# Performance work log

Measured on AMD Instinct MI355X. Metric: run time of the kernel, lower is better.

Reference implementation:

```python
import jax, jax.numpy as jnp
import numpy as np

C = 256
CQK = C // 8  # 32

def setup_inputs() -> dict:
    key = jax.random.key(0)
    ks = jax.random.split(key, 8)
    B, H, W = 8, 64, 64
    x = jax.random.normal(ks[0], (B, C, H, W), dtype=jnp.float32)
    y = jax.random.normal(ks[1], (B, C, H, W), dtype=jnp.float32)
    s = 1.0 / np.sqrt(C)
    Wq = jax.random.normal(ks[2], (CQK, C), dtype=jnp.float32) * s
    bq = jnp.zeros((CQK,), dtype=jnp.float32)
    Wk = jax.random.normal(ks[3], (CQK, C), dtype=jnp.float32) * s
    bk = jnp.zeros((CQK,), dtype=jnp.float32)
    Wv = jax.random.normal(ks[4], (C, C), dtype=jnp.float32) * s
    bv = jnp.zeros((C,), dtype=jnp.float32)
    return {"x": x, "y": y, "Wq": Wq, "bq": bq, "Wk": Wk, "bk": bk, "Wv": Wv, "bv": bv}

def reference(x, y, Wq, bq, Wk, bk, Wv, bv):
    B, Cc, H, W = x.shape
    HW = H * W
    xf = x.reshape(B, Cc, HW)  # [B,C,HW]
    yf = y.reshape(B, Cc, HW)
    # 1x1 convs == per-pixel linear projections
    Q = jnp.einsum('oc,bcn->bno', Wq, xf) + bq          # [B,HW,CQK]
    K = jnp.einsum('oc,bcn->bon', Wk, yf) + bk[:, None]  # [B,CQK,HW]
    V = jnp.einsum('oc,bcn->bon', Wv, yf) + bv[:, None]  # [B,C,HW]
    attn = jax.nn.softmax(jnp.einsum('bnd,bdm->bnm', Q, K), axis=-1)  # [B,HW,HW]
    out = jnp.einsum('bcm,bnm->bcn', V, attn)  # V @ attn^T -> [B,C,HW]
    return out.reshape(B, Cc, H, W)
```

## Files before the change

kernel.cpp:

```cpp
#include <hip/hip_runtime.h>

typedef unsigned short u16;
typedef _Float16 f16;
typedef __attribute__((ext_vector_type(8))) short v8s;
typedef __attribute__((ext_vector_type(4))) short v4s;
typedef __attribute__((ext_vector_type(8))) f16   v8h;
typedef __attribute__((ext_vector_type(4))) float v4f;
typedef __attribute__((ext_vector_type(16))) float v16f;
typedef __attribute__((ext_vector_type(4))) unsigned v4u;

#define NB   8
#define NC   256
#define DQK  32
#define NPIX 4096

__device__ __forceinline__ u16 f2bf(float f) {
  unsigned u = __builtin_bit_cast(unsigned, f);
  u += 0x7FFFu + ((u >> 16) & 1u);
  return (u16)(u >> 16);
}
__device__ __forceinline__ u16 f2h(float f) {
  return __builtin_bit_cast(u16, (f16)f);
}
__device__ __forceinline__ unsigned cvt_pk_bf16(float lo, float hi) {
  unsigned r;
  asm("v_cvt_pk_bf16_f32 %0, %1, %2" : "=v"(r) : "v"(lo), "v"(hi));
  return r;
}
__device__ __forceinline__ float fast_exp2(float x) {
  float r;
  asm("v_exp_f32 %0, %1" : "=v"(r) : "v"(x));
  return r;
}

__global__ __launch_bounds__(256)
void convert_w(const float* __restrict__ Wq, const float* __restrict__ Wk,
               const float* __restrict__ Wv,
               u16* __restrict__ Whq, u16* __restrict__ Whk, u16* __restrict__ Whv) {
  int i = blockIdx.x * 256 + threadIdx.x;
  if (i < 8192)       Whq[i]         = f2h(Wq[i]);
  else if (i < 16384) Whk[i - 8192]  = f2h(Wk[i - 8192]);
  else                Whv[i - 16384] = f2h(Wv[i - 16384]);
}

__global__ __launch_bounds__(256, 2)
void proj_direct(const float* __restrict__ x, const float* __restrict__ y,
                 const u16* __restrict__ Whq, const float* __restrict__ bq,
                 const u16* __restrict__ Whk, const float* __restrict__ bk,
                 const u16* __restrict__ Whv, const float* __restrict__ bv,
                 u16* __restrict__ Qb, u16* __restrict__ Kb, u16* __restrict__ Vt) {
  const int tid = threadIdx.x, w = tid >> 6, lane = tid & 63;
  const int lr = lane & 15, quad = lane >> 4;
  const int b = blockIdx.x & 7;
  const int n0 = (blockIdx.x >> 3) * 64;
  const int n = n0 + w * 16 + lr;
  const size_t bn = ((size_t)b << 12) + n;

  const float* __restrict__ xp = x + ((size_t)b << 20) + n;
  const float* __restrict__ yp = y + ((size_t)b << 20) + n;

  v4f aq[2], ak[2], av[16];
#pragma unroll
  for (int ot = 0; ot < 2; ++ot) { aq[ot] = (v4f){0.f,0.f,0.f,0.f}; ak[ot] = (v4f){0.f,0.f,0.f,0.f}; }
#pragma unroll
  for (int vt = 0; vt < 16; ++vt) av[vt] = (v4f){0.f,0.f,0.f,0.f};

#pragma unroll
  for (int cs = 0; cs < 4; ++cs) {
    v8h xb0, xb1, yb0, yb1;
#pragma unroll
    for (int j = 0; j < 8; ++j) {
      const size_t c0 = (size_t)(cs * 64 + quad * 8 + j) * NPIX;
      const size_t c1 = (size_t)(cs * 64 + 32 + quad * 8 + j) * NPIX;
      xb0[j] = (f16)xp[c0];
      xb1[j] = (f16)xp[c1];
      yb0[j] = (f16)yp[c0];
      yb1[j] = (f16)yp[c1];
    }

#pragma unroll
    for (int ot = 0; ot < 2; ++ot) {
      const u16* wqp = Whq + (ot * 16 + lr) * 256 + cs * 64 + quad * 8;
      const u16* wkp = Whk + (ot * 16 + lr) * 256 + cs * 64 + quad * 8;
      aq[ot] = __builtin_amdgcn_mfma_f32_16x16x32_f16(*(const v8h*)(wqp),      xb0, aq[ot], 0, 0, 0);
      aq[ot] = __builtin_amdgcn_mfma_f32_16x16x32_f16(*(const v8h*)(wqp + 32), xb1, aq[ot], 0, 0, 0);
      ak[ot] = __builtin_amdgcn_mfma_f32_16x16x32_f16(*(const v8h*)(wkp),      yb0, ak[ot], 0, 0, 0);
      ak[ot] = __builtin_amdgcn_mfma_f32_16x16x32_f16(*(const v8h*)(wkp + 32), yb1, ak[ot], 0, 0, 0);
    }
#pragma unroll
    for (int vt = 0; vt < 16; ++vt) {
      const u16* wvp = Whv + (vt * 16 + lr) * 256 + cs * 64 + quad * 8;
      av[vt] = __builtin_amdgcn_mfma_f32_16x16x32_f16(*(const v8h*)(wvp),      yb0, av[vt], 0, 0, 0);
      av[vt] = __builtin_amdgcn_mfma_f32_16x16x32_f16(*(const v8h*)(wvp + 32), yb1, av[vt], 0, 0, 0);
    }
  }

#pragma unroll
  for (int ot = 0; ot < 2; ++ot) {
    v4f bqv = *(const v4f*)(bq + ot * 16 + quad * 4);
    v4f bkv = *(const v4f*)(bk + ot * 16 + quad * 4);
    v4s q4, k4;
#pragma unroll
    for (int r = 0; r < 4; ++r) {
      q4[r] = (short)f2h(aq[ot][r] + bqv[r]);
      k4[r] = (short)f2h(ak[ot][r] + bkv[r]);
    }
    *(v4s*)(Qb + bn * DQK + ot * 16 + quad * 4) = q4;
    *(v4s*)(Kb + bn * DQK + ot * 16 + quad * 4) = k4;
  }

#pragma unroll
  for (int vt = 0; vt < 16; ++vt) {
#pragma unroll
    for (int r = 0; r < 4; ++r) {
      int o = vt * 16 + quad * 4 + r;
      size_t off = ((((size_t)b * 64 + (n >> 6)) * 32 + (o >> 5) * 4 + ((n >> 4) & 3)) * 64
                    + ((n >> 3) & 1) * 32 + (o & 31)) * 8 + (n & 7);
      Vt[off] = f2bf(av[vt][r] + bv[o]);
    }
  }
}

#define L2E  1.44269504f
#define SHFT -48.0f

#define PACK_TILE(S, PBLO, PBHI)                                              \
  {                                                                           \
    float e0  = fast_exp2(fmaf(S[0],  L2E, SHFT));                            \
    float e1  = fast_exp2(fmaf(S[1],  L2E, SHFT));                            \
    float e2  = fast_exp2(fmaf(S[2],  L2E, SHFT));                            \
    float e3  = fast_exp2(fmaf(S[3],  L2E, SHFT));                            \
    float e4  = fast_exp2(fmaf(S[4],  L2E, SHFT));                            \
    float e5  = fast_exp2(fmaf(S[5],  L2E, SHFT));                            \
    float e6  = fast_exp2(fmaf(S[6],  L2E, SHFT));                            \
    float e7  = fast_exp2(fmaf(S[7],  L2E, SHFT));                            \
    float e8  = fast_exp2(fmaf(S[8],  L2E, SHFT));                            \
    float e9  = fast_exp2(fmaf(S[9],  L2E, SHFT));                            \
    float e10 = fast_exp2(fmaf(S[10], L2E, SHFT));                            \
    float e11 = fast_exp2(fmaf(S[11], L2E, SHFT));                            \
    float e12 = fast_exp2(fmaf(S[12], L2E, SHFT));                            \
    float e13 = fast_exp2(fmaf(S[13], L2E, SHFT));                            \
    float e14 = fast_exp2(fmaf(S[14], L2E, SHFT));                            \
    float e15 = fast_exp2(fmaf(S[15], L2E, SHFT));                            \
    lsum += (((e0 + e1) + (e2 + e3)) + ((e4 + e5) + (e6 + e7)))               \
          + (((e8 + e9) + (e10 + e11)) + ((e12 + e13) + (e14 + e15)));        \
    unsigned u00 = cvt_pk_bf16(e0,  e1),  u01 = cvt_pk_bf16(e2,  e3);         \
    unsigned u10 = cvt_pk_bf16(e4,  e5),  u11 = cvt_pk_bf16(e6,  e7);         \
    unsigned u20 = cvt_pk_bf16(e8,  e9),  u21 = cvt_pk_bf16(e10, e11);        \
    unsigned u30 = cvt_pk_bf16(e12, e13), u31 = cvt_pk_bf16(e14, e15);        \
    asm("v_permlane32_swap_b32 %0, %1" : "+v"(u00), "+v"(u10));               \
    asm("v_permlane32_swap_b32 %0, %1" : "+v"(u01), "+v"(u11));               \
    asm("v_permlane32_swap_b32 %0, %1" : "+v"(u20), "+v"(u30));               \
    asm("v_permlane32_swap_b32 %0, %1" : "+v"(u21), "+v"(u31));               \
    PBLO = __builtin_bit_cast(v8s, (v4u){u00, u01, u10, u11});                \
    PBHI = __builtin_bit_cast(v8s, (v4u){u20, u21, u30, u31});                \
  }

__global__ __launch_bounds__(512, 2)
void attn_kernel(const u16* __restrict__ Qb, const u16* __restrict__ Kb,
                 const u16* __restrict__ Vt, float* __restrict__ out) {
  __shared__ __attribute__((aligned(16))) u16 Vb[4][32][64][8];
  __shared__ float Ls2[4][32];

  const int tid  = threadIdx.x;
  const int w    = tid >> 6;
  const int lane = tid & 63;
  const int l31  = lane & 31;
  const int wq   = w & 3;
  const int g    = w >> 2;
  const int bufbase = g * 2;

  const int b  = blockIdx.x & 7;
  const int q0 = (blockIdx.x >> 3) << 7;
  const int qw = q0 + wq * 32;

  const int h = lane >> 5;
  const u16* Qp = Qb + ((size_t)b * NPIX + qw + l31) * DQK + h * 8;
  const v8h qf0 = *(const v8h*)(Qp);
  const v8h qf1 = *(const v8h*)(Qp + 16);

  const u16* Kp = Kb + ((size_t)b * NPIX + l31) * DQK + h * 8 + (size_t)g * 32 * 2048;

  const u16* Vg = Vt + ((size_t)b << 20) + (size_t)lane * 8 + (size_t)g * 32 * 16384;

  v16f acc[8];
#pragma unroll
  for (int i = 0; i < 8; ++i) acc[i] = (v16f){};
  float lsum = 0.f;
  const v16f vz = (v16f){};

#pragma unroll
  for (int j = 0; j < 8; ++j) {
    const int f = wq * 8 + j;
    __builtin_amdgcn_global_load_lds(
        (const __attribute__((address_space(1))) unsigned*)(Vg + (size_t)f * 512),
        (__attribute__((address_space(3))) unsigned*)(&Vb[bufbase][f][0][0]), 16, 0, 0);
  }
  v8h kc0 = *(const v8h*)(Kp);
  v8h kc1 = *(const v8h*)(Kp + 16);
  v8h kc2 = *(const v8h*)(Kp + 1024);
  v8h kc3 = *(const v8h*)(Kp + 1040);
  v8h kn0 = kc0, kn1 = kc1, kn2 = kc2, kn3 = kc3;

  v8s pB0, pB1, pB2, pB3;
  {
    v16f sA = __builtin_amdgcn_mfma_f32_32x32x16_f16(kc0, qf0, vz, 0, 0, 0);
    sA = __builtin_amdgcn_mfma_f32_32x32x16_f16(kc1, qf1, sA, 0, 0, 0);
    v16f sB = __builtin_amdgcn_mfma_f32_32x32x16_f16(kc2, qf0, vz, 0, 0, 0);
    sB = __builtin_amdgcn_mfma_f32_32x32x16_f16(kc3, qf1, sB, 0, 0, 0);
    PACK_TILE(sA, pB0, pB1);
    PACK_TILE(sB, pB2, pB3);
  }
  {
    const u16* kp1 = Kp + 2048;
    kc0 = *(const v8h*)(kp1);
    kc1 = *(const v8h*)(kp1 + 16);
    kc2 = *(const v8h*)(kp1 + 1024);
    kc3 = *(const v8h*)(kp1 + 1040);
  }

#pragma unroll 1
  for (int it = 0; it < 32; ++it) {
    const int pp = it & 1;
    __builtin_amdgcn_sched_barrier(0);
    if (it < 31) {
      asm volatile("s_waitcnt vmcnt(4)" ::: "memory");
    } else {
      asm volatile("s_waitcnt vmcnt(0)" ::: "memory");
    }
    __builtin_amdgcn_s_barrier();
    __builtin_amdgcn_sched_barrier(0);

    if (it < 31) {
#pragma unroll
      for (int j = 0; j < 8; ++j) {
        const int f = wq * 8 + j;
        __builtin_amdgcn_global_load_lds(
            (const __attribute__((address_space(1))) unsigned*)(Vg + ((size_t)(it + 1) * 32 + f) * 512),
            (__attribute__((address_space(3))) unsigned*)(&Vb[bufbase + (pp ^ 1)][f][0][0]), 16, 0, 0);
      }
    }

    __builtin_amdgcn_s_setprio(1);
#pragma unroll
    for (int ct = 0; ct < 8; ++ct) {
      v8s vf0 = *(const v8s*)(&Vb[bufbase + pp][ct * 4 + 0][lane][0]);
      v8s vf1 = *(const v8s*)(&Vb[bufbase + pp][ct * 4 + 1][lane][0]);
      v8s vf2 = *(const v8s*)(&Vb[bufbase + pp][ct * 4 + 2][lane][0]);
      v8s vf3 = *(const v8s*)(&Vb[bufbase + pp][ct * 4 + 3][lane][0]);
      acc[ct] = __builtin_amdgcn_mfma_f32_32x32x16_bf16(vf0, pB0, acc[ct], 0, 0, 0);
      acc[ct] = __builtin_amdgcn_mfma_f32_32x32x16_bf16(vf1, pB1, acc[ct], 0, 0, 0);
      acc[ct] = __builtin_amdgcn_mfma_f32_32x32x16_bf16(vf2, pB2, acc[ct], 0, 0, 0);
      acc[ct] = __builtin_amdgcn_mfma_f32_32x32x16_bf16(vf3, pB3, acc[ct], 0, 0, 0);
    }
    __builtin_amdgcn_s_setprio(0);

    if (it < 31) {
      v16f sA = __builtin_amdgcn_mfma_f32_32x32x16_f16(kc0, qf0, vz, 0, 0, 0);
      sA = __builtin_amdgcn_mfma_f32_32x32x16_f16(kc1, qf1, sA, 0, 0, 0);
      v16f sB = __builtin_amdgcn_mfma_f32_32x32x16_f16(kc2, qf0, vz, 0, 0, 0);
      sB = __builtin_amdgcn_mfma_f32_32x32x16_f16(kc3, qf1, sB, 0, 0, 0);
      if (it < 30) {
        const u16* kp2 = Kp + (size_t)(it + 2) * 2048;
        kn0 = *(const v8h*)(kp2);
        kn1 = *(const v8h*)(kp2 + 16);
        kn2 = *(const v8h*)(kp2 + 1024);
        kn3 = *(const v8h*)(kp2 + 1040);
      }
      PACK_TILE(sA, pB0, pB1);
      PACK_TILE(sB, pB2, pB3);
      kc0 = kn0; kc1 = kn1; kc2 = kn2; kc3 = kn3;
    }
  }

  lsum += __shfl_xor(lsum, 32);

  __syncthreads();
  float* Cb = (float*)&Vb[0][0][0][0];
  if (w >= 4) {
    const int w4 = w - 4;
#pragma unroll
    for (int ct = 0; ct < 8; ++ct)
#pragma unroll
      for (int k = 0; k < 4; ++k) {
        v4f c = {acc[ct][k * 4 + 0], acc[ct][k * 4 + 1],
                 acc[ct][k * 4 + 2], acc[ct][k * 4 + 3]};
        *(v4f*)(Cb + (((w4 * 32 + ct * 4 + k) * 64 + lane) << 2)) = c;
      }
    if (lane < 32) Ls2[w4][l31] = lsum;
  }
  __syncthreads();
  if (w < 4) {
    const float linv = 1.0f / (lsum + Ls2[w][l31]);
#pragma unroll
    for (int ct = 0; ct < 8; ++ct)
#pragma unroll
      for (int k = 0; k < 4; ++k) {
        v4f c = *(const v4f*)(Cb + (((w * 32 + ct * 4 + k) * 64 + lane) << 2));
        acc[ct][k * 4 + 0] += c[0]; acc[ct][k * 4 + 1] += c[1];
        acc[ct][k * 4 + 2] += c[2]; acc[ct][k * 4 + 3] += c[3];
      }

    float* op = out + (size_t)b * NC * NPIX + q0 + wq * 32 + l31;
#pragma unroll
    for (int ct = 0; ct < 8; ++ct)
#pragma unroll
      for (int r = 0; r < 16; ++r) {
        const int ch = ct * 32 + (r & 3) + ((r >> 2) << 3) + (h << 2);
        op[(size_t)ch * NPIX] = acc[ct][r] * linv;
      }
  }
}

extern "C" void kernel_launch(void* const* d_in, const int* in_sizes, int n_in,
                              void* d_out, int out_size, void* d_ws, size_t ws_size,
                              hipStream_t stream) {
  const float* x  = (const float*)d_in[0];
  const float* y  = (const float*)d_in[1];
  const float* Wq = (const float*)d_in[2];
  const float* bq = (const float*)d_in[3];
  const float* Wk = (const float*)d_in[4];
  const float* bk = (const float*)d_in[5];
  const float* Wv = (const float*)d_in[6];
  const float* bv = (const float*)d_in[7];
  float* out = (float*)d_out;

  u16* Qb  = (u16*)d_ws;
  u16* Kb  = Qb + (size_t)NB * NPIX * DQK;
  u16* Vt  = Kb + (size_t)NB * NPIX * DQK;
  u16* Whq = Vt + (size_t)NB * NC * NPIX;
  u16* Whk = Whq + 32 * 256;
  u16* Whv = Whk + 32 * 256;

  hipLaunchKernelGGL(convert_w, dim3(320), dim3(256), 0, stream, Wq, Wk, Wv, Whq, Whk, Whv);
  hipLaunchKernelGGL(proj_direct, dim3(512), dim3(256), 0, stream,
                     x, y, Whq, bq, Whk, bk, Whv, bv, Qb, Kb, Vt);
  hipLaunchKernelGGL(attn_kernel, dim3(256), dim3(512), 0, stream, Qb, Kb, Vt, out);
}
```

Baseline: 239.3 us.

## Halve attention block to 64 queries and 32-key steps, doubling grid

Result: slower. 261.6 us (+9.3%).

```diff
diff --git a/kernel.cpp b/kernel.cpp
--- a/kernel.cpp
+++ b/kernel.cpp
@@ -156,30 +156,41 @@
     PBHI = __builtin_bit_cast(v8s, (v4u){u20, u21, u30, u31});                \
   }
 
-__global__ __launch_bounds__(512, 2)
+#define STAGE(IT, BUF)                                                        \
+  {                                                                           \
+    _Pragma("unroll")                                                         \
+    for (int j = 0; j < 8; ++j) {                                             \
+      const size_t f = (size_t)wq * 16 + ((j >> 1) << 2) + (((IT) & 1) << 1) + (j & 1); \
+      __builtin_amdgcn_global_load_lds(                                       \
+          (const __attribute__((address_space(1))) unsigned*)(Vg + (((size_t)((IT) >> 1) * 32) + f) * 512), \
+          (__attribute__((address_space(3))) unsigned*)(&SB[BUF][wq * 8 + j][0][0]), 16, 0, 0); \
+    }                                                                         \
+  }
+
+__global__ __launch_bounds__(256, 2)
 void attn_kernel(const u16* __restrict__ Qb, const u16* __restrict__ Kb,
                  const u16* __restrict__ Vt, float* __restrict__ out) {
-  __shared__ __attribute__((aligned(16))) u16 Vb[4][32][64][8];
-  __shared__ float Ls2[4][32];
+  __shared__ __attribute__((aligned(16))) u16 SB[4][16][64][8];
+  __shared__ float Ls2[2][32];
 
   const int tid  = threadIdx.x;
   const int w    = tid >> 6;
   const int lane = tid & 63;
   const int l31  = lane & 31;
-  const int wq   = w & 3;
-  const int g    = w >> 2;
+  const int h    = lane >> 5;
+  const int wq   = w & 1;
+  const int g    = w >> 1;
   const int bufbase = g * 2;
 
   const int b  = blockIdx.x & 7;
-  const int q0 = (blockIdx.x >> 3) << 7;
+  const int q0 = (blockIdx.x >> 3) << 6;
   const int qw = q0 + wq * 32;
 
-  const int h = lane >> 5;
   const u16* Qp = Qb + ((size_t)b * NPIX + qw + l31) * DQK + h * 8;
   const v8h qf0 = *(const v8h*)(Qp);
   const v8h qf1 = *(const v8h*)(Qp + 16);
 
-  const u16* Kp = Kb + ((size_t)b * NPIX + l31) * DQK + h * 8 + (size_t)g * 32 * 2048;
+  const u16* Kp = Kb + ((size_t)b * NPIX + l31) * DQK + h * 8 + (size_t)g * 2048 * DQK;
 
   const u16* Vg = Vt + ((size_t)b << 20) + (size_t)lane * 8 + (size_t)g * 32 * 16384;
 
@@ -189,108 +200,77 @@
   float lsum = 0.f;
   const v16f vz = (v16f){};
 
-#pragma unroll
-  for (int j = 0; j < 8; ++j) {
-    const int f = wq * 8 + j;
-    __builtin_amdgcn_global_load_lds(
-        (const __attribute__((address_space(1))) unsigned*)(Vg + (size_t)f * 512),
-        (__attribute__((address_space(3))) unsigned*)(&Vb[bufbase][f][0][0]), 16, 0, 0);
-  }
-  v8h kc0 = *(const v8h*)(Kp);
-  v8h kc1 = *(const v8h*)(Kp + 16);
-  v8h kc2 = *(const v8h*)(Kp + 1024);
-  v8h kc3 = *(const v8h*)(Kp + 1040);
-  v8h kn0 = kc0, kn1 = kc1, kn2 = kc2, kn3 = kc3;
-
-  v8s pB0, pB1, pB2, pB3;
+  v8h kc0, kc1, kn0, kn1;
+  v8s pB0, pB1;
   {
-    v16f sA = __builtin_amdgcn_mfma_f32_32x32x16_f16(kc0, qf0, vz, 0, 0, 0);
-    sA = __builtin_amdgcn_mfma_f32_32x32x16_f16(kc1, qf1, sA, 0, 0, 0);
-    v16f sB = __builtin_amdgcn_mfma_f32_32x32x16_f16(kc2, qf0, vz, 0, 0, 0);
-    sB = __builtin_amdgcn_mfma_f32_32x32x16_f16(kc3, qf1, sB, 0, 0, 0);
+    v8h t0 = *(const v8h*)(Kp);
+    v8h t1 = *(const v8h*)(Kp + 16);
+    STAGE(0, bufbase);
+    v16f sA = __builtin_amdgcn_mfma_f32_32x32x16_f16(t0, qf0, vz, 0, 0, 0);
+    sA = __builtin_amdgcn_mfma_f32_32x32x16_f16(t1, qf1, sA, 0, 0, 0);
     PACK_TILE(sA, pB0, pB1);
-    PACK_TILE(sB, pB2, pB3);
-  }
-  {
-    const u16* kp1 = Kp + 2048;
-    kc0 = *(const v8h*)(kp1);
-    kc1 = *(const v8h*)(kp1 + 16);
-    kc2 = *(const v8h*)(kp1 + 1024);
-    kc3 = *(const v8h*)(kp1 + 1040);
+    kc0 = *(const v8h*)(Kp + 1024);
+    kc1 = *(const v8h*)(Kp + 1040);
+    kn0 = kc0; kn1 = kc1;
   }
 
 #pragma unroll 1
-  for (int it = 0; it < 32; ++it) {
+  for (int it = 0; it < 64; ++it) {
     const int pp = it & 1;
     __builtin_amdgcn_sched_barrier(0);
-    if (it < 31) {
-      asm volatile("s_waitcnt vmcnt(4)" ::: "memory");
+    if (it < 63) {
+      asm volatile("s_waitcnt vmcnt(2)" ::: "memory");
     } else {
       asm volatile("s_waitcnt vmcnt(0)" ::: "memory");
     }
     __builtin_amdgcn_s_barrier();
     __builtin_amdgcn_sched_barrier(0);
 
-    if (it < 31) {
-#pragma unroll
-      for (int j = 0; j < 8; ++j) {
-        const int f = wq * 8 + j;
-        __builtin_amdgcn_global_load_lds(
-            (const __attribute__((address_space(1))) unsigned*)(Vg + ((size_t)(it + 1) * 32 + f) * 512),
-            (__attribute__((address_space(3))) unsigned*)(&Vb[bufbase + (pp ^ 1)][f][0][0]), 16, 0, 0);
-      }
+    if (it < 63) {
+      STAGE(it + 1, bufbase + (pp ^ 1));
     }
 
     __builtin_amdgcn_s_setprio(1);
 #pragma unroll
     for (int ct = 0; ct < 8; ++ct) {
-      v8s vf0 = *(const v8s*)(&Vb[bufbase + pp][ct * 4 + 0][lane][0]);
-      v8s vf1 = *(const v8s*)(&Vb[bufbase + pp][ct * 4 + 1][lane][0]);
-      v8s vf2 = *(const v8s*)(&Vb[bufbase + pp][ct * 4 + 2][lane][0]);
-      v8s vf3 = *(const v8s*)(&Vb[bufbase + pp][ct * 4 + 3][lane][0]);
+      v8s vf0 = *(const v8s*)(&SB[bufbase + pp][ct * 2 + 0][lane][0]);
+      v8s vf1 = *(const v8s*)(&SB[bufbase + pp][ct * 2 + 1][lane][0]);
       acc[ct] = __builtin_amdgcn_mfma_f32_32x32x16_bf16(vf0, pB0, acc[ct], 0, 0, 0);
       acc[ct] = __builtin_amdgcn_mfma_f32_32x32x16_bf16(vf1, pB1, acc[ct], 0, 0, 0);
-      acc[ct] = __builtin_amdgcn_mfma_f32_32x32x16_bf16(vf2, pB2, acc[ct], 0, 0, 0);
-      acc[ct] = __builtin_amdgcn_mfma_f32_32x32x16_bf16(vf3, pB3, acc[ct], 0, 0, 0);
     }
     __builtin_amdgcn_s_setprio(0);
 
-    if (it < 31) {
+    if (it < 63) {
       v16f sA = __builtin_amdgcn_mfma_f32_32x32x16_f16(kc0, qf0, vz, 0, 0, 0);
       sA = __builtin_amdgcn_mfma_f32_32x32x16_f16(kc1, qf1, sA, 0, 0, 0);
-      v16f sB = __builtin_amdgcn_mfma_f32_32x32x16_f16(kc2, qf0, vz, 0, 0, 0);
-      sB = __builtin_amdgcn_mfma_f32_32x32x16_f16(kc3, qf1, sB, 0, 0, 0);
-      if (it < 30) {
-        const u16* kp2 = Kp + (size_t)(it + 2) * 2048;
+      if (it < 62) {
+        const u16* kp2 = Kp + (size_t)(it + 2) * 1024;
         kn0 = *(const v8h*)(kp2);
         kn1 = *(const v8h*)(kp2 + 16);
-        kn2 = *(const v8h*)(kp2 + 1024);
-        kn3 = *(const v8h*)(kp2 + 1040);
       }
       PACK_TILE(sA, pB0, pB1);
-      PACK_TILE(sB, pB2, pB3);
-      kc0 = kn0; kc1 = kn1; kc2 = kn2; kc3 = kn3;
+      kc0 = kn0; kc1 = kn1;
     }
   }
 
   lsum += __shfl_xor(lsum, 32);
 
   __syncthreads();
-  float* Cb = (float*)&Vb[0][0][0][0];
-  if (w >= 4) {
-    const int w4 = w - 4;
+  float* Cb = (float*)&SB[0][0][0][0];
+  if (w >= 2) {
+    const int w2 = w - 2;
 #pragma unroll
     for (int ct = 0; ct < 8; ++ct)
 #pragma unroll
       for (int k = 0; k < 4; ++k) {
         v4f c = {acc[ct][k * 4 + 0], acc[ct][k * 4 + 1],
                  acc[ct][k * 4 + 2], acc[ct][k * 4 + 3]};
-        *(v4f*)(Cb + (((w4 * 32 + ct * 4 + k) * 64 + lane) << 2)) = c;
+        *(v4f*)(Cb + (((w2 * 32 + ct * 4 + k) * 64 + lane) << 2)) = c;
       }
-    if (lane < 32) Ls2[w4][l31] = lsum;
+    if (lane < 32) Ls2[w2][l31] = lsum;
   }
   __syncthreads();
-  if (w < 4) {
+  if (w < 2) {
     const float linv = 1.0f / (lsum + Ls2[w][l31]);
 #pragma unroll
     for (int ct = 0; ct < 8; ++ct)
@@ -301,7 +281,7 @@
         acc[ct][k * 4 + 2] += c[2]; acc[ct][k * 4 + 3] += c[3];
       }
 
-    float* op = out + (size_t)b * NC * NPIX + q0 + wq * 32 + l31;
+    float* op = out + (size_t)b * NC * NPIX + q0 + w * 32 + l31;
 #pragma unroll
     for (int ct = 0; ct < 8; ++ct)
 #pragma unroll
@@ -335,5 +315,5 @@
   hipLaunchKernelGGL(convert_w, dim3(320), dim3(256), 0, stream, Wq, Wk, Wv, Whq, Whk, Whv);
   hipLaunchKernelGGL(proj_direct, dim3(512), dim3(256), 0, stream,
                      x, y, Whq, bq, Whk, bk, Whv, bv, Qb, Kb, Vt);
-  hipLaunchKernelGGL(attn_kernel, dim3(256), dim3(512), 0, stream, Qb, Kb, Vt, out);
-}
+  hipLaunchKernelGGL(attn_kernel, dim3(512), dim3(256), 0, stream, Qb, Kb, Vt, out);
+}
```
